# Kernel optimization log

Measured on AMD Instinct MI355X. Metric: run time of the kernel, lower is better.

Reference implementation:

```python
import jax, jax.numpy as jnp
import numpy as np

NUM_ITER = 3  # routing iterations (canonical CapsNet)
EPS = 1e-12


def _conv(x, w, stride):
    return jax.lax.conv_general_dilated(
        x, w, (stride, stride), 'VALID',
        dimension_numbers=('NCHW', 'OIHW', 'NCHW'))


def _squash(t, axis=-1):
    sn = (t * t).sum(axis=axis, keepdims=True)
    return sn / (1.0 + sn) * t / jnp.sqrt(sn + EPS)


def _batchnorm(x, eps=1e-5):
    # fresh BatchNorm2d in training mode: batch stats, weight=1, bias=0, biased var
    m = x.mean((0, 2, 3), keepdims=True)
    v = ((x - m) ** 2).mean((0, 2, 3), keepdims=True)
    return (x - m) * jax.lax.rsqrt(v + eps)


def _branch(x, cw, cb, pw, pb, rw):
    # x: [B,1,H,W]; cw: [128,1,k,k]; pw: [8,32,128,k,k]; rw: [10,R,8,16]
    y = jax.nn.relu(_conv(x, cw, 1) + cb[None, :, None, None])
    y = _batchnorm(y)
    nc, oc = pw.shape[0], pw.shape[1]  # 8 capsules, 32 channels each
    p = _conv(y, pw.reshape(nc * oc, pw.shape[2], pw.shape[3], pw.shape[4]), 2)
    p = p + pb.reshape(-1)[None, :, None, None]          # [B,256,h,w]
    B = p.shape[0]
    u = jnp.transpose(p.reshape(B, nc, -1), (0, 2, 1))   # [B,R,8], R=32*h*w
    u = _squash(u, axis=-1)
    priors = jnp.einsum('bri,nrio->nbro', u, rw)         # [10,B,R,16]
    b = jnp.zeros(priors.shape[:3] + (1,), priors.dtype)  # [10,B,R,1]
    for i in range(NUM_ITER):
        c = jax.nn.softmax(b, axis=2)                    # over route nodes
        v = _squash((c * priors).sum(axis=2, keepdims=True))  # [10,B,1,16]
        if i < NUM_ITER - 1:
            b = b + (priors * v).sum(axis=-1, keepdims=True)
    v = jnp.transpose(v[:, :, 0, :], (1, 0, 2))          # [B,10,16]
    return jnp.sqrt((v * v).sum(-1) + EPS)               # [B,10] capsule lengths


def setup_inputs() -> dict:
    key = jax.random.key(0)
    ks = jax.random.split(key, 16)
    s = 0.05
    return {
        'x': jax.random.normal(ks[0], (256, 1, 28, 28), jnp.float32),
        'conv1_w': jax.random.normal(ks[1], (128, 1, 3, 3), jnp.float32) * s,
        'conv1_b': jnp.zeros((128,), jnp.float32),
        'prim1_w': jax.random.normal(ks[2], (8, 32, 128, 3, 3), jnp.float32) * s,
        'prim1_b': jnp.zeros((8, 32), jnp.float32),
        'digit1_w': jax.random.normal(ks[3], (10, 128, 8, 16), jnp.float32),
        'conv2_w': jax.random.normal(ks[4], (128, 1, 5, 5), jnp.float32) * s,
        'conv2_b': jnp.zeros((128,), jnp.float32),
        'prim2_w': jax.random.normal(ks[5], (8, 32, 128, 5, 5), jnp.float32) * s,
        'prim2_b': jnp.zeros((8, 32), jnp.float32),
        'digit2_w': jax.random.normal(ks[6], (10, 288, 8, 16), jnp.float32),
        'conv3_w': jax.random.normal(ks[7], (128, 1, 9, 9), jnp.float32) * s,
        'conv3_b': jnp.zeros((128,), jnp.float32),
        'prim3_w': jax.random.normal(ks[8], (8, 32, 128, 9, 9), jnp.float32) * s,
        'prim3_b': jnp.zeros((8, 32), jnp.float32),
        'digit3_w': jax.random.normal(ks[9], (10, 1152, 8, 16), jnp.float32),
    }


def reference(x, conv1_w, conv1_b, prim1_w, prim1_b, digit1_w,
              conv2_w, conv2_b, prim2_w, prim2_b, digit2_w,
              conv3_w, conv3_b, prim3_w, prim3_b, digit3_w):
    img = x[:, 0]                                   # [B,28,28]
    B = img.shape[0]
    x3 = img                                        # 28x28
    x2 = img.reshape(B, 14, 2, 14, 2).mean((2, 4))  # 14x14 pyramid level
    x1 = x2.reshape(B, 7, 2, 7, 2).mean((2, 4))     # 7x7 pyramid level
    l1 = _branch(x1[:, None], conv1_w, conv1_b, prim1_w, prim1_b, digit1_w)
    l2 = _branch(x2[:, None], conv2_w, conv2_b, prim2_w, prim2_b, digit2_w)
    l3 = _branch(x3[:, None], conv3_w, conv3_b, prim3_w, prim3_b, digit3_w)
    return jax.nn.softmax(l1 + l2 + l3, axis=-1)    # [B,10]
```

## Files before the change

kernel.cpp:

```cpp
#include <hip/hip_runtime.h>
#include <math.h>

#define SQ_EPS 1e-12f
#define BN_EPS 1e-5f

typedef short short8 __attribute__((ext_vector_type(8)));
typedef float f32x4 __attribute__((ext_vector_type(4)));
typedef unsigned short ushort_t;

__device__ inline unsigned short f2bf(float x) {
    unsigned int u = __float_as_uint(x);
    unsigned int r = (u + 0x7fffu + ((u >> 16) & 1u)) >> 16;
    return (unsigned short)r;
}
__device__ inline float bf2f(unsigned short h) {
    return __uint_as_float(((unsigned int)h) << 16);
}

template<int IH, int IW, int KS, int OH, int OW>
__device__ void conv_body(const float* __restrict__ w, const float* __restrict__ bias,
                          ushort_t* __restrict__ yh, ushort_t* __restrict__ yl,
                          float* __restrict__ partial,
                          int b, int tid, float* s_img, float* s_w, float* s_red) {
    constexpr int KK = KS * KS;
    constexpr int OS = OH * OW;
    for (int i = tid; i < 128 * KK; i += 256) s_w[i] = w[i];
    __syncthreads();
    int c = tid & 127, half = tid >> 7;
    float bias_c = bias[c];
    float bsum = 0.f, bsq = 0.f;
    for (int r = half; r < OH; r += 2) {
        float acc[OW];
        #pragma unroll
        for (int j = 0; j < OW; ++j) acc[j] = bias_c;
        for (int u = 0; u < KS; ++u) {
            float rg[OW + KS - 1];
            #pragma unroll
            for (int j = 0; j < OW + KS - 1; ++j) rg[j] = s_img[(r + u) * IW + j];
            #pragma unroll
            for (int v = 0; v < KS; ++v) {
                float wv = s_w[c * KK + u * KS + v];
                #pragma unroll
                for (int j = 0; j < OW; ++j) acc[j] += wv * rg[j + v];
            }
        }
        #pragma unroll
        for (int j = 0; j < OW; ++j) {
            float val = fmaxf(acc[j], 0.f);
            bsum += val; bsq += val * val;
            unsigned short h = f2bf(val);
            unsigned short lo = f2bf(val - bf2f(h));
            int oidx = ((b * OS) + r * OW + j) * 128 + c;
            yh[oidx] = h; yl[oidx] = lo;
        }
    }
    s_red[tid] = bsum; __syncthreads();
    if (tid < 128) partial[b * 256 + c] = s_red[tid] + s_red[tid + 128];
    __syncthreads();
    s_red[tid] = bsq; __syncthreads();
    if (tid < 128) partial[b * 256 + 128 + c] = s_red[tid] + s_red[tid + 128];
}

__global__ __launch_bounds__(256) void conv_all_kernel(
        const float* __restrict__ img,
        const float* __restrict__ c1w, const float* __restrict__ c1b,
        const float* __restrict__ c2w, const float* __restrict__ c2b,
        const float* __restrict__ c3w, const float* __restrict__ c3b,
        ushort_t* __restrict__ yh1, ushort_t* __restrict__ yl1,
        ushort_t* __restrict__ yh2, ushort_t* __restrict__ yl2,
        ushort_t* __restrict__ yh3, ushort_t* __restrict__ yl3,
        float* __restrict__ partial_base) {
    __shared__ float s_img[784];
    __shared__ float s_tmp[196];
    __shared__ float s_w[128 * 81];
    __shared__ float s_red[256];
    int br = blockIdx.x >> 8, b = blockIdx.x & 255, tid = threadIdx.x;
    const float* im = img + b * 784;
    for (int i = tid; i < 784; i += 256) s_img[i] = im[i];
    __syncthreads();
    if (br <= 1) {
        for (int idx = tid; idx < 196; idx += 256) {
            int i = idx / 14, j = idx % 14;
            s_tmp[idx] = 0.25f * (s_img[(2*i)*28 + 2*j]   + s_img[(2*i)*28 + 2*j + 1] +
                                  s_img[(2*i+1)*28 + 2*j] + s_img[(2*i+1)*28 + 2*j + 1]);
        }
        __syncthreads();
        if (br == 0) {
            for (int idx = tid; idx < 49; idx += 256) {
                int i = idx / 7, j = idx % 7;
                s_img[idx] = 0.25f * (s_tmp[(2*i)*14 + 2*j]   + s_tmp[(2*i)*14 + 2*j + 1] +
                                      s_tmp[(2*i+1)*14 + 2*j] + s_tmp[(2*i+1)*14 + 2*j + 1]);
            }
        } else {
            for (int idx = tid; idx < 196; idx += 256) s_img[idx] = s_tmp[idx];
        }
        __syncthreads();
    }
    if (br == 0)      conv_body<7, 7, 3, 5, 5>(c1w, c1b, yh1, yl1, partial_base, b, tid, s_img, s_w, s_red);
    else if (br == 1) conv_body<14, 14, 5, 10, 10>(c2w, c2b, yh2, yl2, partial_base + 65536, b, tid, s_img, s_w, s_red);
    else              conv_body<28, 28, 9, 20, 20>(c3w, c3b, yh3, yl3, partial_base + 131072, b, tid, s_img, s_w, s_red);
}

__global__ void bn_final_kernel(const float* __restrict__ partial_base, float* __restrict__ bnp_base) {
    int br = blockIdx.x;
    const float* pp = partial_base + br * 65536;
    float* bnp = bnp_base + br * 512;
    float N = (br == 0) ? 6400.f : ((br == 1) ? 25600.f : 102400.f);
    int c = threadIdx.x;
    float s = 0.f, q = 0.f;
    for (int blk = 0; blk < 256; ++blk) {
        s += pp[blk * 256 + c];
        q += pp[blk * 256 + 128 + c];
    }
    float mean = s / N;
    float var = q / N - mean * mean;
    float inv = rsqrtf(var + BN_EPS);
    bnp[256 + c] = inv;
    bnp[384 + c] = -mean * inv;
}

__global__ __launch_bounds__(256) void wtrans_zero_kernel(
        const float* __restrict__ w1, const float* __restrict__ w2,
        const float* __restrict__ w3, const float* __restrict__ bnp_base,
        const float* __restrict__ pb1, const float* __restrict__ pb2,
        const float* __restrict__ pb3,
        ushort_t* __restrict__ wh1, ushort_t* __restrict__ wl1,
        ushort_t* __restrict__ wh2, ushort_t* __restrict__ wl2,
        ushort_t* __restrict__ wh3, ushort_t* __restrict__ wl3,
        float* __restrict__ b1, float* __restrict__ b2, float* __restrict__ b3,
        float* __restrict__ p3zero) {
    __shared__ float tile[128 * 81];
    __shared__ float r2[2];
    int blk = blockIdx.x, tid = threadIdx.x;
    if (blk >= 768) {
        ((float4*)p3zero)[(blk - 768) * 256 + tid] = (float4){0.f, 0.f, 0.f, 0.f};
        return;
    }
    int br = blk >> 8, ch = blk & 255;
    const float* w; const float* pb; ushort_t* wh; ushort_t* wl; float* bf; int KK;
    if (br == 0)      { w = w1; pb = pb1; wh = wh1; wl = wl1; bf = b1; KK = 9;  }
    else if (br == 1) { w = w2; pb = pb2; wh = wh2; wl = wl2; bf = b2; KK = 25; }
    else              { w = w3; pb = pb3; wh = wh3; wl = wl3; bf = b3; KK = 81; }
    const float* bnp = bnp_base + br * 512;
    int n = 128 * KK;
    const float* wrow = w + ch * n;
    for (int i = tid; i < n; i += 256) tile[i] = wrow[i];
    __syncthreads();
    for (int j = tid; j < n; j += 256) {
        int uv = j >> 7, c = j & 127;
        float val = tile[c * KK + uv] * bnp[256 + c];
        unsigned short h = f2bf(val);
        unsigned short lo = f2bf(val - bf2f(h));
        int oidx = uv * 32768 + (ch << 7) + c;
        wh[oidx] = h; wl[oidx] = lo;
    }
    float s = 0.f;
    if (tid < 128) {
        for (int uv = 0; uv < KK; ++uv) s += tile[tid * KK + uv];
        s *= bnp[384 + tid];
    }
    for (int off = 32; off; off >>= 1) s += __shfl_down(s, off);
    if (tid < 128 && (tid & 63) == 0) r2[tid >> 6] = s;
    __syncthreads();
    if (tid == 0) bf[ch] = pb[ch] + r2[0] + r2[1];
}

template<int S, int WO, int IHg, int IWg, int KS, int ZCH>
__device__ void gemm_body(const ushort_t* __restrict__ yh, const ushort_t* __restrict__ yl,
                          const ushort_t* __restrict__ wh, const ushort_t* __restrict__ wl,
                          float* __restrict__ p, int bx, int by, int bz, int tid,
                          ushort_t* Ash, ushort_t* Asl, ushort_t* Bsh, ushort_t* Bsl) {
    int bm = bx * 128, ch0 = by * 128;
    int arow = tid >> 2;
    int c0 = tid & 3;
    int sw0 = (c0 ^ ((arow >> 1) & 3)) * 8;
    int wA0 = arow * 32 + sw0;
    int wA1 = (arow + 64) * 32 + sw0;
    int m0 = bm + arow;
    int b0 = m0 / S, s0 = m0 % S;
    int abase0 = ((b0 * IHg + 2 * (s0 / WO)) * IWg + 2 * (s0 % WO)) * 128 + c0 * 8;
    int m1 = m0 + 64;
    int b1 = m1 / S, s1 = m1 % S;
    int abase1 = ((b1 * IHg + 2 * (s1 / WO)) * IWg + 2 * (s1 % WO)) * 128 + c0 * 8;
    int bbase0 = (ch0 + arow) * 128 + c0 * 8;
    int bbase1 = (ch0 + arow + 64) * 128 + c0 * 8;
    int lane = tid & 63, wid = tid >> 6;
    int wm = wid & 1, wn = wid >> 1;
    int quad = lane >> 4, l16 = lane & 15;
    int aoffL[4], boffL[4];
    #pragma unroll
    for (int mi = 0; mi < 4; ++mi) {
        int row = wm * 64 + mi * 16 + l16;
        aoffL[mi] = row * 32 + ((quad ^ ((row >> 1) & 3)) * 8);
    }
    #pragma unroll
    for (int ni = 0; ni < 4; ++ni) {
        int row = wn * 64 + ni * 16 + l16;
        boffL[ni] = row * 32 + ((quad ^ ((row >> 1) & 3)) * 8);
    }
    f32x4 acc[4][4];
    #pragma unroll
    for (int mi = 0; mi < 4; ++mi)
        #pragma unroll
        for (int ni = 0; ni < 4; ++ni)
            acc[mi][ni] = (f32x4){0.f, 0.f, 0.f, 0.f};

    int kc = bz * ZCH;
    int uv = kc >> 2, ci = kc & 3;
    int u = uv / KS, v = uv - u * KS;
    int aoff = (u * IWg + v) * 128 + (ci << 5);
    int boff = uv * 32768 + (ci << 5);
    int4 a0h = *reinterpret_cast<const int4*>(yh + abase0 + aoff);
    int4 a0l = *reinterpret_cast<const int4*>(yl + abase0 + aoff);
    int4 a1h = *reinterpret_cast<const int4*>(yh + abase1 + aoff);
    int4 a1l = *reinterpret_cast<const int4*>(yl + abase1 + aoff);
    int4 b0h = *reinterpret_cast<const int4*>(wh + bbase0 + boff);
    int4 b0l = *reinterpret_cast<const int4*>(wl + bbase0 + boff);
    int4 b1h = *reinterpret_cast<const int4*>(wh + bbase1 + boff);
    int4 b1l = *reinterpret_cast<const int4*>(wl + bbase1 + boff);

    for (int t = 0; t < ZCH; ++t) {
        __syncthreads();
        *reinterpret_cast<int4*>(&Ash[wA0]) = a0h;
        *reinterpret_cast<int4*>(&Asl[wA0]) = a0l;
        *reinterpret_cast<int4*>(&Ash[wA1]) = a1h;
        *reinterpret_cast<int4*>(&Asl[wA1]) = a1l;
        *reinterpret_cast<int4*>(&Bsh[wA0]) = b0h;
        *reinterpret_cast<int4*>(&Bsl[wA0]) = b0l;
        *reinterpret_cast<int4*>(&Bsh[wA1]) = b1h;
        *reinterpret_cast<int4*>(&Bsl[wA1]) = b1l;
        if (t + 1 < ZCH) {
            ci = (ci + 1) & 3;
            if (ci == 0) { ++uv; ++v; if (v == KS) { v = 0; ++u; } }
            aoff = (u * IWg + v) * 128 + (ci << 5);
            boff = uv * 32768 + (ci << 5);
            a0h = *reinterpret_cast<const int4*>(yh + abase0 + aoff);
            a0l = *reinterpret_cast<const int4*>(yl + abase0 + aoff);
            a1h = *reinterpret_cast<const int4*>(yh + abase1 + aoff);
            a1l = *reinterpret_cast<const int4*>(yl + abase1 + aoff);
            b0h = *reinterpret_cast<const int4*>(wh + bbase0 + boff);
            b0l = *reinterpret_cast<const int4*>(wl + bbase0 + boff);
            b1h = *reinterpret_cast<const int4*>(wh + bbase1 + boff);
            b1l = *reinterpret_cast<const int4*>(wl + bbase1 + boff);
        }
        __syncthreads();
        short8 bh[4], bl[4];
        #pragma unroll
        for (int ni = 0; ni < 4; ++ni) {
            bh[ni] = *reinterpret_cast<const short8*>(&Bsh[boffL[ni]]);
            bl[ni] = *reinterpret_cast<const short8*>(&Bsl[boffL[ni]]);
        }
        #pragma unroll
        for (int mi = 0; mi < 4; ++mi) {
            short8 ah = *reinterpret_cast<const short8*>(&Ash[aoffL[mi]]);
            short8 al = *reinterpret_cast<const short8*>(&Asl[aoffL[mi]]);
            #pragma unroll
            for (int ni = 0; ni < 4; ++ni) {
                acc[mi][ni] = __builtin_amdgcn_mfma_f32_16x16x32_bf16(ah, bh[ni], acc[mi][ni], 0, 0, 0);
                acc[mi][ni] = __builtin_amdgcn_mfma_f32_16x16x32_bf16(al, bh[ni], acc[mi][ni], 0, 0, 0);
                acc[mi][ni] = __builtin_amdgcn_mfma_f32_16x16x32_bf16(ah, bl[ni], acc[mi][ni], 0, 0, 0);
            }
        }
    }
    #pragma unroll
    for (int mi = 0; mi < 4; ++mi)
        #pragma unroll
        for (int ni = 0; ni < 4; ++ni) {
            int col = ch0 + wn * 64 + ni * 16 + l16;
            #pragma unroll
            for (int reg = 0; reg < 4; ++reg) {
                int row = bm + wm * 64 + mi * 16 + quad * 4 + reg;
                atomicAdd(p + (size_t)row * 256 + col, acc[mi][ni][reg]);
            }
        }
}

__global__ __launch_bounds__(256, 3) void gemm3_kernel(
        const ushort_t* __restrict__ yh, const ushort_t* __restrict__ yl,
        const ushort_t* __restrict__ wh, const ushort_t* __restrict__ wl,
        float* __restrict__ p) {
    __shared__ ushort_t Ash[128 * 32], Asl[128 * 32];
    __shared__ ushort_t Bsh[128 * 32], Bsl[128 * 32];
    gemm_body<36, 6, 20, 20, 9, 54>(yh, yl, wh, wl, p,
                                    blockIdx.x, blockIdx.y, blockIdx.z, threadIdx.x,
                                    Ash, Asl, Bsh, Bsl);
}

__global__ __launch_bounds__(256, 3) void gemm21_kernel(
        const ushort_t* __restrict__ yh2, const ushort_t* __restrict__ yl2,
        const ushort_t* __restrict__ wh2, const ushort_t* __restrict__ wl2, float* __restrict__ p2,
        const ushort_t* __restrict__ yh1, const ushort_t* __restrict__ yl1,
        const ushort_t* __restrict__ wh1, const ushort_t* __restrict__ wl1, float* __restrict__ p1) {
    __shared__ ushort_t Ash[128 * 32], Asl[128 * 32];
    __shared__ ushort_t Bsh[128 * 32], Bsl[128 * 32];
    int blk = blockIdx.x, tid = threadIdx.x;
    if (blk < 360) {
        int z = blk / 36, rem = blk % 36, y = rem / 18, x = rem % 18;
        gemm_body<9, 3, 10, 10, 5, 10>(yh2, yl2, wh2, wl2, p2, x, y, z, tid, Ash, Asl, Bsh, Bsl);
    } else {
        int b = blk - 360;
        int z = b / 16, rem = b % 16, y = rem / 8, x = rem % 8;
        gemm_body<4, 2, 5, 5, 3, 4>(yh1, yl1, wh1, wl1, p1, x, y, z, tid, Ash, Asl, Bsh, Bsl);
    }
}

__global__ void squash_all_kernel(const float* __restrict__ p1, const float* __restrict__ p2,
                                  const float* __restrict__ p3,
                                  const float* __restrict__ bias1, const float* __restrict__ bias2,
                                  const float* __restrict__ bias3,
                                  float* __restrict__ u1, float* __restrict__ u2,
                                  float* __restrict__ u3) {
    int blk = blockIdx.x;
    const float* p; const float* bias; float* u; int S;
    if (blk < 128)      { p = p1; bias = bias1; u = u1; S = 4; }
    else if (blk < 416) { p = p2; bias = bias2; u = u2; S = 9;  blk -= 128; }
    else                { p = p3; bias = bias3; u = u3; S = 36; blk -= 416; }
    int idx = blk * 256 + threadIdx.x;
    int o = idx & 31, rest = idx >> 5;
    int s = rest % S, b = rest / S;
    const float* pp = p + (size_t)(b * S + s) * 256 + o;
    float t[8]; float sn = 0.f;
    #pragma unroll
    for (int i = 0; i < 8; ++i) { t[i] = pp[i * 32] + bias[o + i * 32]; sn += t[i] * t[i]; }
    float f = sn / ((1.f + sn) * sqrtf(sn + SQ_EPS));
    float* up = u + (size_t)(b * (32 * S) + o * S + s) * 8;
    float4 w0 = {t[0] * f, t[1] * f, t[2] * f, t[3] * f};
    float4 w1 = {t[4] * f, t[5] * f, t[6] * f, t[7] * f};
    *reinterpret_cast<float4*>(up) = w0;
    *reinterpret_cast<float4*>(up + 4) = w1;
}

__global__ void rwtrans_zero_kernel(const float* __restrict__ w1, const float* __restrict__ w2,
                                    const float* __restrict__ w3,
                                    ushort_t* __restrict__ o1, ushort_t* __restrict__ o2,
                                    ushort_t* __restrict__ o3,
                                    float* __restrict__ p2, float* __restrict__ p1) {
    int blk = blockIdx.x;
    if (blk >= 7840) {
        int zb = blk - 7840;
        if (zb < 576) ((float4*)p2)[zb * 256 + threadIdx.x] = (float4){0.f, 0.f, 0.f, 0.f};
        else          ((float4*)p1)[(zb - 576) * 256 + threadIdx.x] = (float4){0.f, 0.f, 0.f, 0.f};
        return;
    }
    int idx = blk * 256 + threadIdx.x;
    if (idx < 163840) {
        int t = idx;
        int jj = t & 7; t >>= 3;
        int r = t & 127; t >>= 7;
        int g = t & 15; int n = t >> 4;
        o1[idx] = f2bf(w1[(n * 128 + r) * 128 + g * 8 + jj]);
    } else if (idx < 532480) {
        int t = idx - 163840;
        int jj = t & 7; t >>= 3;
        int r = t % 288; t /= 288;
        int g = t & 15; int n = t >> 4;
        o2[idx - 163840] = f2bf(w2[(n * 288 + r) * 128 + g * 8 + jj]);
    } else {
        int t = idx - 532480;
        int jj = t & 7; t >>= 3;
        int r = t % 1152; t /= 1152;
        int g = t & 15; int n = t >> 4;
        o3[idx - 532480] = f2bf(w3[(n * 1152 + r) * 128 + g * 8 + jj]);
    }
}

template<int R>
__device__ void routing_body(const float* __restrict__ u, const ushort_t* __restrict__ rwb,
                             float* __restrict__ lens, int n, int b, int tid,
                             unsigned int* pri, float* red, float* vsh, float* sred) {
    constexpr int KMAX = (R + 255) / 256;
    int lane = tid & 63, wv = tid >> 6;
    #pragma unroll
    for (int k = 0; k < KMAX; ++k) {
        int r = tid + k * 256;
        if (r < R) {
            const float4* up = (const float4*)(u + ((size_t)b * R + r) * 8);
            float4 ua = up[0], ub2 = up[1];
            float uu[8] = {ua.x, ua.y, ua.z, ua.w, ub2.x, ub2.y, ub2.z, ub2.w};
            float po[16] = {};
            #pragma unroll
            for (int g = 0; g < 16; ++g) {
                short8 wg = *reinterpret_cast<const short8*>(rwb + (((size_t)n * 16 + g) * R + r) * 8);
                float ui = uu[g >> 1];
                int o0 = (g & 1) * 8;
                #pragma unroll
                for (int jj = 0; jj < 8; ++jj)
                    po[o0 + jj] += ui * bf2f((unsigned short)wg[jj]);
            }
            #pragma unroll
            for (int j = 0; j < 8; ++j)
                pri[j * R + r] = (unsigned int)f2bf(po[2*j]) | ((unsigned int)f2bf(po[2*j+1]) << 16);
        }
    }
    __syncthreads();
    float v[16];
    float blog[KMAX];
    #pragma unroll
    for (int k = 0; k < KMAX; ++k) blog[k] = 0.f;
    {
        float sacc[16] = {};
        #pragma unroll
        for (int k = 0; k < KMAX; ++k) {
            int r = tid + k * 256;
            if (r < R) {
                #pragma unroll
                for (int j = 0; j < 8; ++j) {
                    unsigned int w = pri[j * R + r];
                    sacc[2*j]   += bf2f((unsigned short)(w & 0xffffu));
                    sacc[2*j+1] += bf2f((unsigned short)(w >> 16));
                }
            }
        }
        #pragma unroll
        for (int o = 0; o < 16; ++o) {
            float xv = sacc[o];
            for (int off = 32; off; off >>= 1) xv += __shfl_down(xv, off);
            if (lane == 0) red[wv * 16 + o] = xv;
        }
        __syncthreads();
        if (tid < 16) vsh[tid] = (red[tid] + red[16 + tid] + red[32 + tid] + red[48 + tid]) * (1.0f / (float)R);
        __syncthreads();
        if (tid == 0) {
            float sn = 0.f;
            #pragma unroll
            for (int o = 0; o < 16; ++o) sn += vsh[o] * vsh[o];
            float f = sn / ((1.f + sn) * sqrtf(sn + SQ_EPS));
            #pragma unroll
            for (int o = 0; o < 16; ++o) vsh[o] *= f;
        }
        __syncthreads();
        #pragma unroll
        for (int o = 0; o < 16; ++o) v[o] = vsh[o];
        __syncthreads();
    }
    for (int it = 0; it < 2; ++it) {
        float sacc[16] = {};
        float lsum = 0.f;
        #pragma unroll
        for (int k = 0; k < KMAX; ++k) {
            int r = tid + k * 256;
            if (r < R) {
                float pv[16];
                #pragma unroll
                for (int j = 0; j < 8; ++j) {
                    unsigned int w = pri[j * R + r];
                    pv[2*j]   = bf2f((unsigned short)(w & 0xffffu));
                    pv[2*j+1] = bf2f((unsigned short)(w >> 16));
                }
                float dot = 0.f;
                #pragma unroll
                for (int o = 0; o < 16; ++o) dot += pv[o] * v[o];
                blog[k] += dot;
                float e = expf(blog[k]);
                lsum += e;
                #pragma unroll
                for (int o = 0; o < 16; ++o) sacc[o] += e * pv[o];
            }
        }
        for (int off = 32; off; off >>= 1) lsum += __shfl_down(lsum, off);
        if (lane == 0) sred[wv] = lsum;
        #pragma unroll
        for (int o = 0; o < 16; ++o) {
            float xv = sacc[o];
            for (int off = 32; off; off >>= 1) xv += __shfl_down(xv, off);
            if (lane == 0) red[wv * 16 + o] = xv;
        }
        __syncthreads();
        if (tid < 16) {
            float tot = sred[0] + sred[1] + sred[2] + sred[3];
            vsh[tid] = (red[tid] + red[16 + tid] + red[32 + tid] + red[48 + tid]) / tot;
        }
        __syncthreads();
        if (tid == 0) {
            float sn = 0.f;
            #pragma unroll
            for (int o = 0; o < 16; ++o) sn += vsh[o] * vsh[o];
            float f = sn / ((1.f + sn) * sqrtf(sn + SQ_EPS));
            #pragma unroll
            for (int o = 0; o < 16; ++o) vsh[o] *= f;
        }
        __syncthreads();
        #pragma unroll
        for (int o = 0; o < 16; ++o) v[o] = vsh[o];
        __syncthreads();
    }
    if (tid == 0) {
        float sn = 0.f;
        #pragma unroll
        for (int o = 0; o < 16; ++o) sn += v[o] * v[o];
        lens[b * 10 + n] = sqrtf(sn + SQ_EPS);
    }
}

__global__ __launch_bounds__(256, 4) void routing_all_kernel(
        const float* __restrict__ u1, const float* __restrict__ u2, const float* __restrict__ u3,
        const ushort_t* __restrict__ rwb1, const ushort_t* __restrict__ rwb2,
        const ushort_t* __restrict__ rwb3,
        float* __restrict__ l1, float* __restrict__ l2, float* __restrict__ l3) {
    __shared__ unsigned int pri[8 * 1152];
    __shared__ float red[4 * 16];
    __shared__ float vsh[16];
    __shared__ float sred[4];
    int n = blockIdx.x, b = blockIdx.y, br = blockIdx.z, tid = threadIdx.x;
    if (br == 0)      routing_body<128>(u1, rwb1, l1, n, b, tid, pri, red, vsh, sred);
    else if (br == 1) routing_body<288>(u2, rwb2, l2, n, b, tid, pri, red, vsh, sred);
    else              routing_body<1152>(u3, rwb3, l3, n, b, tid, pri, red, vsh, sred);
}

__global__ void final_softmax_kernel(const float* __restrict__ l1, const float* __restrict__ l2,
                                     const float* __restrict__ l3, float* __restrict__ out) {
    int b = threadIdx.x;
    float v[10]; float mx = -1e30f;
    #pragma unroll
    for (int n = 0; n < 10; ++n) {
        v[n] = l1[b * 10 + n] + l2[b * 10 + n] + l3[b * 10 + n];
        mx = fmaxf(mx, v[n]);
    }
    float s = 0.f;
    #pragma unroll
    for (int n = 0; n < 10; ++n) { v[n] = expf(v[n] - mx); s += v[n]; }
    float inv = 1.f / s;
    #pragma unroll
    for (int n = 0; n < 10; ++n) out[b * 10 + n] = v[n] * inv;
}

extern "C" void kernel_launch(void* const* d_in, const int* in_sizes, int n_in,
                              void* d_out, int out_size, void* d_ws, size_t ws_size,
                              hipStream_t stream) {
    const float* x   = (const float*)d_in[0];
    const float* c1w = (const float*)d_in[1];
    const float* c1b = (const float*)d_in[2];
    const float* p1w = (const float*)d_in[3];
    const float* p1b = (const float*)d_in[4];
    const float* d1w = (const float*)d_in[5];
    const float* c2w = (const float*)d_in[6];
    const float* c2b = (const float*)d_in[7];
    const float* p2w = (const float*)d_in[8];
    const float* p2b = (const float*)d_in[9];
    const float* d2w = (const float*)d_in[10];
    const float* c3w = (const float*)d_in[11];
    const float* c3b = (const float*)d_in[12];
    const float* p3w = (const float*)d_in[13];
    const float* p3b = (const float*)d_in[14];
    const float* d3w = (const float*)d_in[15];

    float* ws = (float*)d_ws;
    float* yh1f  = ws + 62720;
    float* yl1f  = ws + 472320;
    float* yh2f  = ws + 881920;
    float* yl2f  = ws + 2520320;
    float* yh3f  = ws + 4158720;
    float* yl3f  = ws + 10712320;
    float* wh1f  = ws + 17265920;
    float* wl1f  = ws + 17413376;
    float* wh2f  = ws + 17560832;
    float* wl2f  = ws + 17970432;
    float* wh3f  = ws + 18380032;
    float* wl3f  = ws + 19707136;
    float* p3    = ws + 21034240;
    float* bnp1  = ws + 23393536;
    float* bias1 = ws + 23395072;
    float* bias2 = ws + 23395328;
    float* bias3 = ws + 23395584;
    float* l1    = ws + 23395840;
    float* l2    = ws + 23398400;
    float* l3    = ws + 23400960;

    ushort_t* yh1 = (ushort_t*)yh1f; ushort_t* yl1 = (ushort_t*)yl1f;
    ushort_t* yh2 = (ushort_t*)yh2f; ushort_t* yl2 = (ushort_t*)yl2f;
    ushort_t* yh3 = (ushort_t*)yh3f; ushort_t* yl3 = (ushort_t*)yl3f;
    ushort_t* wh1 = (ushort_t*)wh1f; ushort_t* wl1 = (ushort_t*)wl1f;
    ushort_t* wh2 = (ushort_t*)wh2f; ushort_t* wl2 = (ushort_t*)wl2f;
    ushort_t* wh3 = (ushort_t*)wh3f; ushort_t* wl3 = (ushort_t*)wl3f;
    float* u1 = yh1f;
    float* u2 = yh2f;
    float* u3 = yh3f;
    float* p2 = wh3f;
    float* p1 = wl3f;
    ushort_t* rwb1 = (ushort_t*)yl3f;
    ushort_t* rwb2 = rwb1 + 163840;
    ushort_t* rwb3 = rwb2 + 368640;

    conv_all_kernel<<<768, 256, 0, stream>>>(x, c1w, c1b, c2w, c2b, c3w, c3b,
                                             yh1, yl1, yh2, yl2, yh3, yl3, p3);
    bn_final_kernel<<<3, 128, 0, stream>>>(p3, bnp1);
    wtrans_zero_kernel<<<3072, 256, 0, stream>>>(p1w, p2w, p3w, bnp1, p1b, p2b, p3b,
                                                 wh1, wl1, wh2, wl2, wh3, wl3,
                                                 bias1, bias2, bias3, p3);
    gemm3_kernel<<<dim3(72, 2, 6), 256, 0, stream>>>(yh3, yl3, wh3, wl3, p3);
    rwtrans_zero_kernel<<<8672, 256, 0, stream>>>(d1w, d2w, d3w, rwb1, rwb2, rwb3, p2, p1);
    gemm21_kernel<<<504, 256, 0, stream>>>(yh2, yl2, wh2, wl2, p2, yh1, yl1, wh1, wl1, p1);
    squash_all_kernel<<<1568, 256, 0, stream>>>(p1, p2, p3, bias1, bias2, bias3, u1, u2, u3);
    routing_all_kernel<<<dim3(10, 256, 3), 256, 0, stream>>>(u1, u2, u3, rwb1, rwb2, rwb3, l1, l2, l3);
    final_softmax_kernel<<<1, 256, 0, stream>>>(l1, l2, l3, (float*)d_out);
}
```

Before: 555.8 us.

## Keep routing weights fp32, vectorize priors LDS layout, schedule largest branch first

The digit routing weights are now transposed into an fp32 layout grouped by four outputs instead of being converted to bf16 in groups of eight. Priors in shared memory move from a strided per-j layout to a per-route-node contiguous layout, with the two 16-byte halves swapped on odd nodes to spread bank accesses, so each thread uses two uint4 LDS accesses. The branch index is reversed so the heavy R=1152 blocks are dispatched first. This doubles the global bytes read for weights, and the fp32 weights must still fit in the reused workspace buffer.

New measurement: 532.5 us. 1.04x faster.

```diff
diff --git a/kernel.cpp b/kernel.cpp
--- a/kernel.cpp
+++ b/kernel.cpp
@@ -332,8 +332,8 @@
 
 __global__ void rwtrans_zero_kernel(const float* __restrict__ w1, const float* __restrict__ w2,
                                     const float* __restrict__ w3,
-                                    ushort_t* __restrict__ o1, ushort_t* __restrict__ o2,
-                                    ushort_t* __restrict__ o3,
+                                    float* __restrict__ o1, float* __restrict__ o2,
+                                    float* __restrict__ o3,
                                     float* __restrict__ p2, float* __restrict__ p1) {
     int blk = blockIdx.x;
     if (blk >= 7840) {
@@ -345,27 +345,27 @@
     int idx = blk * 256 + threadIdx.x;
     if (idx < 163840) {
         int t = idx;
-        int jj = t & 7; t >>= 3;
+        int jj = t & 3; t >>= 2;
         int r = t & 127; t >>= 7;
-        int g = t & 15; int n = t >> 4;
-        o1[idx] = f2bf(w1[(n * 128 + r) * 128 + g * 8 + jj]);
+        int g2 = t & 31; int n = t >> 5;
+        o1[idx] = w1[(n * 128 + r) * 128 + g2 * 4 + jj];
     } else if (idx < 532480) {
         int t = idx - 163840;
-        int jj = t & 7; t >>= 3;
+        int jj = t & 3; t >>= 2;
         int r = t % 288; t /= 288;
-        int g = t & 15; int n = t >> 4;
-        o2[idx - 163840] = f2bf(w2[(n * 288 + r) * 128 + g * 8 + jj]);
+        int g2 = t & 31; int n = t >> 5;
+        o2[idx - 163840] = w2[(n * 288 + r) * 128 + g2 * 4 + jj];
     } else {
         int t = idx - 532480;
-        int jj = t & 7; t >>= 3;
+        int jj = t & 3; t >>= 2;
         int r = t % 1152; t /= 1152;
-        int g = t & 15; int n = t >> 4;
-        o3[idx - 532480] = f2bf(w3[(n * 1152 + r) * 128 + g * 8 + jj]);
+        int g2 = t & 31; int n = t >> 5;
+        o3[idx - 532480] = w3[(n * 1152 + r) * 128 + g2 * 4 + jj];
     }
 }
 
 template<int R>
-__device__ void routing_body(const float* __restrict__ u, const ushort_t* __restrict__ rwb,
+__device__ void routing_body(const float* __restrict__ u, const float* __restrict__ rwt,
                              float* __restrict__ lens, int n, int b, int tid,
                              unsigned int* pri, float* red, float* vsh, float* sred) {
     constexpr int KMAX = (R + 255) / 256;
@@ -379,17 +379,23 @@
             float uu[8] = {ua.x, ua.y, ua.z, ua.w, ub2.x, ub2.y, ub2.z, ub2.w};
             float po[16] = {};
             #pragma unroll
-            for (int g = 0; g < 16; ++g) {
-                short8 wg = *reinterpret_cast<const short8*>(rwb + (((size_t)n * 16 + g) * R + r) * 8);
-                float ui = uu[g >> 1];
-                int o0 = (g & 1) * 8;
-                #pragma unroll
-                for (int jj = 0; jj < 8; ++jj)
-                    po[o0 + jj] += ui * bf2f((unsigned short)wg[jj]);
+            for (int g2 = 0; g2 < 32; ++g2) {
+                float4 w4 = *reinterpret_cast<const float4*>(rwt + (((size_t)n * 32 + g2) * R + r) * 4);
+                float ui = uu[g2 >> 2];
+                int o0 = (g2 & 3) * 4;
+                po[o0 + 0] += ui * w4.x;
+                po[o0 + 1] += ui * w4.y;
+                po[o0 + 2] += ui * w4.z;
+                po[o0 + 3] += ui * w4.w;
             }
+            unsigned int d[8];
             #pragma unroll
             for (int j = 0; j < 8; ++j)
-                pri[j * R + r] = (unsigned int)f2bf(po[2*j]) | ((unsigned int)f2bf(po[2*j+1]) << 16);
+                d[j] = (unsigned int)f2bf(po[2*j]) | ((unsigned int)f2bf(po[2*j+1]) << 16);
+            int i0 = r * 8 + ((0 ^ (r & 1)) * 4);
+            int i1 = r * 8 + ((1 ^ (r & 1)) * 4);
+            *reinterpret_cast<uint4*>(pri + i0) = (uint4){d[0], d[1], d[2], d[3]};
+            *reinterpret_cast<uint4*>(pri + i1) = (uint4){d[4], d[5], d[6], d[7]};
         }
     }
     __syncthreads();
@@ -403,11 +409,15 @@
         for (int k = 0; k < KMAX; ++k) {
             int r = tid + k * 256;
             if (r < R) {
+                int i0 = r * 8 + ((0 ^ (r & 1)) * 4);
+                int i1 = r * 8 + ((1 ^ (r & 1)) * 4);
+                uint4 h0 = *reinterpret_cast<const uint4*>(pri + i0);
+                uint4 h1 = *reinterpret_cast<const uint4*>(pri + i1);
+                unsigned int d[8] = {h0.x, h0.y, h0.z, h0.w, h1.x, h1.y, h1.z, h1.w};
                 #pragma unroll
                 for (int j = 0; j < 8; ++j) {
-                    unsigned int w = pri[j * R + r];
-                    sacc[2*j]   += bf2f((unsigned short)(w & 0xffffu));
-                    sacc[2*j+1] += bf2f((unsigned short)(w >> 16));
+                    sacc[2*j]   += bf2f((unsigned short)(d[j] & 0xffffu));
+                    sacc[2*j+1] += bf2f((unsigned short)(d[j] >> 16));
                 }
             }
         }
@@ -440,12 +450,16 @@
         for (int k = 0; k < KMAX; ++k) {
             int r = tid + k * 256;
             if (r < R) {
+                int i0 = r * 8 + ((0 ^ (r & 1)) * 4);
+                int i1 = r * 8 + ((1 ^ (r & 1)) * 4);
+                uint4 h0 = *reinterpret_cast<const uint4*>(pri + i0);
+                uint4 h1 = *reinterpret_cast<const uint4*>(pri + i1);
+                unsigned int d[8] = {h0.x, h0.y, h0.z, h0.w, h1.x, h1.y, h1.z, h1.w};
                 float pv[16];
                 #pragma unroll
                 for (int j = 0; j < 8; ++j) {
-                    unsigned int w = pri[j * R + r];
-                    pv[2*j]   = bf2f((unsigned short)(w & 0xffffu));
-                    pv[2*j+1] = bf2f((unsigned short)(w >> 16));
+                    pv[2*j]   = bf2f((unsigned short)(d[j] & 0xffffu));
+                    pv[2*j+1] = bf2f((unsigned short)(d[j] >> 16));
                 }
                 float dot = 0.f;
                 #pragma unroll
@@ -494,17 +508,17 @@
 
 __global__ __launch_bounds__(256, 4) void routing_all_kernel(
         const float* __restrict__ u1, const float* __restrict__ u2, const float* __restrict__ u3,
-        const ushort_t* __restrict__ rwb1, const ushort_t* __restrict__ rwb2,
-        const ushort_t* __restrict__ rwb3,
+        const float* __restrict__ rwt1, const float* __restrict__ rwt2,
+        const float* __restrict__ rwt3,
         float* __restrict__ l1, float* __restrict__ l2, float* __restrict__ l3) {
     __shared__ unsigned int pri[8 * 1152];
     __shared__ float red[4 * 16];
     __shared__ float vsh[16];
     __shared__ float sred[4];
-    int n = blockIdx.x, b = blockIdx.y, br = blockIdx.z, tid = threadIdx.x;
-    if (br == 0)      routing_body<128>(u1, rwb1, l1, n, b, tid, pri, red, vsh, sred);
-    else if (br == 1) routing_body<288>(u2, rwb2, l2, n, b, tid, pri, red, vsh, sred);
-    else              routing_body<1152>(u3, rwb3, l3, n, b, tid, pri, red, vsh, sred);
+    int n = blockIdx.x, b = blockIdx.y, br = 2 - blockIdx.z, tid = threadIdx.x;
+    if (br == 0)      routing_body<128>(u1, rwt1, l1, n, b, tid, pri, red, vsh, sred);
+    else if (br == 1) routing_body<288>(u2, rwt2, l2, n, b, tid, pri, red, vsh, sred);
+    else              routing_body<1152>(u3, rwt3, l3, n, b, tid, pri, red, vsh, sred);
 }
 
 __global__ void final_softmax_kernel(const float* __restrict__ l1, const float* __restrict__ l2,
@@ -577,9 +591,9 @@
     float* u3 = yh3f;
     float* p2 = wh3f;
     float* p1 = wl3f;
-    ushort_t* rwb1 = (ushort_t*)yl3f;
-    ushort_t* rwb2 = rwb1 + 163840;
-    ushort_t* rwb3 = rwb2 + 368640;
+    float* rwt1 = yl3f;
+    float* rwt2 = rwt1 + 163840;
+    float* rwt3 = rwt2 + 368640;
 
     conv_all_kernel<<<768, 256, 0, stream>>>(x, c1w, c1b, c2w, c2b, c3w, c3b,
                                              yh1, yl1, yh2, yl2, yh3, yl3, p3);
@@ -588,9 +602,9 @@
                                                  wh1, wl1, wh2, wl2, wh3, wl3,
                                                  bias1, bias2, bias3, p3);
     gemm3_kernel<<<dim3(72, 2, 6), 256, 0, stream>>>(yh3, yl3, wh3, wl3, p3);
-    rwtrans_zero_kernel<<<8672, 256, 0, stream>>>(d1w, d2w, d3w, rwb1, rwb2, rwb3, p2, p1);
+    rwtrans_zero_kernel<<<8672, 256, 0, stream>>>(d1w, d2w, d3w, rwt1, rwt2, rwt3, p2, p1);
     gemm21_kernel<<<504, 256, 0, stream>>>(yh2, yl2, wh2, wl2, p2, yh1, yl1, wh1, wl1, p1);
     squash_all_kernel<<<1568, 256, 0, stream>>>(p1, p2, p3, bias1, bias2, bias3, u1, u2, u3);
-    routing_all_kernel<<<dim3(10, 256, 3), 256, 0, stream>>>(u1, u2, u3, rwb1, rwb2, rwb3, l1, l2, l3);
+    routing_all_kernel<<<dim3(10, 256, 3), 256, 0, stream>>>(u1, u2, u3, rwt1, rwt2, rwt3, l1, l2, l3);
     final_softmax_kernel<<<1, 256, 0, stream>>>(l1, l2, l3, (float*)d_out);
 }
```
